# Performance work log

Hardware: AMD Instinct MI355X
Metric: run time of the kernel (lower is better)

Reference implementation:

```python
import jax, jax.numpy as jnp
import numpy as np

IN_F = 8192
OUT_F = 8192
MAX_STATES = 100
THRESHOLD = MAX_STATES // 2  # 50


def setup_inputs() -> dict:
    key = jax.random.key(0)
    k1, k2 = jax.random.split(key, 2)
    spike_input = (jax.random.uniform(k1, (IN_F,)) < 0.2).astype(jnp.float32)
    # synapse states as in __init__: randn*5 + threshold, clamped to [1, max_states]
    synapse_states = jnp.clip(
        jax.random.normal(k2, (OUT_F, IN_F)) * 5.0 + THRESHOLD, 1.0, float(MAX_STATES)
    ).astype(jnp.float32)
    membrane_potential = jnp.zeros((OUT_F,), jnp.float32)
    adaptive_threshold = jnp.full((OUT_F,), 3.0, jnp.float32)
    eligibility_trace = jnp.zeros((OUT_F, IN_F), jnp.float32)
    refractory_period = jnp.zeros((OUT_F,), jnp.float32)
    return {
        "spike_input": spike_input,
        "synapse_states": synapse_states,
        "membrane_potential": membrane_potential,
        "adaptive_threshold": adaptive_threshold,
        "eligibility_trace": eligibility_trace,
        "refractory_period": refractory_period,
    }


def reference(spike_input, synapse_states, membrane_potential, adaptive_threshold,
              eligibility_trace, refractory_period):
    # Ternary (effectively binary 0/1) weights from synapse states
    w = (synapse_states > float(THRESHOLD)).astype(jnp.float32)  # [out, in]
    x = spike_input.reshape(-1)                                   # [in]
    current = w @ x                                               # [out]
    # LIF membrane update with refractory gating
    v_mem = membrane_potential * 0.5 + current * (1.0 - refractory_period * 0.5)
    spikes = (v_mem >= adaptive_threshold).astype(jnp.float32)    # [out]
    # Eligibility trace: decay + outer-product accumulation + clamp
    new_trace = jnp.clip(eligibility_trace * 0.8 + jnp.outer(spikes, x), 0.0, 5.0)
    # Refractory update
    new_refractory = jnp.clip(refractory_period + spikes - 0.1, 0.0, 1.0)
    # Membrane reset where spiked
    new_membrane = v_mem * (1.0 - spikes)
    return spikes, new_membrane, new_trace, new_refractory
```

## Files before the change

### kernel.cpp

```cpp
#include <hip/hip_runtime.h>


#define IN_F 8192
#define OUT_F 8192
#define BLOCK 256

__global__ __launch_bounds__(BLOCK) void snn_matvec_kernel(
    const float4* __restrict__ x4,
    const float* __restrict__ syn,
    const float* __restrict__ mem,
    const float* __restrict__ thr,
    const float* __restrict__ refr,
    float* __restrict__ out_spikes,
    float* __restrict__ out_mem,
    float* __restrict__ out_refr)
{
    const int wave = threadIdx.x >> 6;
    const int lane = threadIdx.x & 63;
    const int row  = (blockIdx.x << 2) + wave;

    const float4* __restrict__ syn4 =
        (const float4*)(syn + (size_t)row * IN_F);

    float acc = 0.0f;
    #pragma unroll 8
    for (int it = 0; it < IN_F / 4 / 64; ++it) {
        const int idx = (it << 6) + lane;
        const float4 s  = syn4[idx];
        const float4 xv = x4[idx];
        acc += (s.x > 50.0f) ? xv.x : 0.0f;
        acc += (s.y > 50.0f) ? xv.y : 0.0f;
        acc += (s.z > 50.0f) ? xv.z : 0.0f;
        acc += (s.w > 50.0f) ? xv.w : 0.0f;
    }
    #pragma unroll
    for (int off = 32; off > 0; off >>= 1) {
        acc += __shfl_down(acc, off, 64);
    }
    if (lane == 0) {
        const float r = refr[row];
        const float v = mem[row] * 0.5f + acc * (1.0f - r * 0.5f);
        const float spike = (v >= thr[row]) ? 1.0f : 0.0f;
        out_spikes[row] = spike;
        out_mem[row]    = v * (1.0f - spike);
        out_refr[row]   = fminf(fmaxf(r + spike - 0.1f, 0.0f), 1.0f);
    }
}

__global__ __launch_bounds__(BLOCK) void snn_trace_kernel(
    const float4* __restrict__ x4,
    const float4* __restrict__ tr4,
    const float* __restrict__ spikes,
    float4* __restrict__ otr4)
{
    const int row = blockIdx.x;
    const float spike = spikes[row];
    const size_t base = (size_t)row * (IN_F / 4);

    #pragma unroll
    for (int it = 0; it < IN_F / 4 / BLOCK; ++it) {
        const int idx = it * BLOCK + threadIdx.x;
        const float4 t  = tr4[base + idx];
        const float4 xv = x4[idx];
        float4 o;
        o.x = fminf(fmaxf(t.x * 0.8f + spike * xv.x, 0.0f), 5.0f);
        o.y = fminf(fmaxf(t.y * 0.8f + spike * xv.y, 0.0f), 5.0f);
        o.z = fminf(fmaxf(t.z * 0.8f + spike * xv.z, 0.0f), 5.0f);
        o.w = fminf(fmaxf(t.w * 0.8f + spike * xv.w, 0.0f), 5.0f);
        otr4[base + idx] = o;
    }
}

extern "C" void kernel_launch(void* const* d_in, const int* in_sizes, int n_in,
                              void* d_out, int out_size, void* d_ws, size_t ws_size,
                              hipStream_t stream) {
    const float* x_in  = (const float*)d_in[0];
    const float* syn   = (const float*)d_in[1];
    const float* mem   = (const float*)d_in[2];
    const float* thr   = (const float*)d_in[3];
    const float* trace = (const float*)d_in[4];
    const float* refr  = (const float*)d_in[5];

    float* out = (float*)d_out;
    float* out_spikes = out;
    float* out_mem    = out + OUT_F;
    float* out_trace  = out + 2 * OUT_F;
    float* out_refr   = out + 2 * OUT_F + (size_t)OUT_F * IN_F;

    snn_matvec_kernel<<<OUT_F / 4, BLOCK, 0, stream>>>(
        (const float4*)x_in, syn, mem, thr, refr,
        out_spikes, out_mem, out_refr);

    snn_trace_kernel<<<OUT_F, BLOCK, 0, stream>>>(
        (const float4*)x_in, (const float4*)trace, out_spikes,
        (float4*)out_trace);
}
```

Measured before the change: 589.6 us.

## Fuse matvec and eligibility-trace update into one kernel with nontemporal accesses

Merges the spike matvec and the trace update into a single kernel in which each wave computes its row's spike, then immediately streams that row's trace. An xor-shuffle reduction gives every lane the spike value, removing the second launch and the global spike round-trip. Synapse and trace streams use nontemporal loads and stores to avoid cache pollution. Each wave now does twice the sequential work, which may reduce memory-level parallelism per row.

```diff
diff --git a/kernel.cpp b/kernel.cpp
--- a/kernel.cpp
+++ b/kernel.cpp
@@ -4,70 +4,68 @@
 #define IN_F 8192
 #define OUT_F 8192
 #define BLOCK 256
+#define CHUNKS (IN_F / 4 / 64)
 
-__global__ __launch_bounds__(BLOCK) void snn_matvec_kernel(
-    const float4* __restrict__ x4,
+typedef float f32x4 __attribute__((ext_vector_type(4)));
+
+__global__ __launch_bounds__(BLOCK) void snn_fused_kernel(
+    const f32x4* __restrict__ x4,
     const float* __restrict__ syn,
     const float* __restrict__ mem,
     const float* __restrict__ thr,
     const float* __restrict__ refr,
+    const f32x4* __restrict__ tr4,
     float* __restrict__ out_spikes,
     float* __restrict__ out_mem,
-    float* __restrict__ out_refr)
+    float* __restrict__ out_refr,
+    f32x4* __restrict__ otr4)
 {
     const int wave = threadIdx.x >> 6;
     const int lane = threadIdx.x & 63;
     const int row  = (blockIdx.x << 2) + wave;
 
-    const float4* __restrict__ syn4 =
-        (const float4*)(syn + (size_t)row * IN_F);
+    const size_t base4 = (size_t)row * (IN_F / 4);
+    const f32x4* __restrict__ syn4 = (const f32x4*)syn + base4;
+
+    const float r_in = refr[row];
+    const float m_in = mem[row];
+    const float t_in = thr[row];
 
     float acc = 0.0f;
     #pragma unroll 8
-    for (int it = 0; it < IN_F / 4 / 64; ++it) {
+    for (int it = 0; it < CHUNKS; ++it) {
         const int idx = (it << 6) + lane;
-        const float4 s  = syn4[idx];
-        const float4 xv = x4[idx];
-        acc += (s.x > 50.0f) ? xv.x : 0.0f;
-        acc += (s.y > 50.0f) ? xv.y : 0.0f;
-        acc += (s.z > 50.0f) ? xv.z : 0.0f;
-        acc += (s.w > 50.0f) ? xv.w : 0.0f;
+        const f32x4 s  = __builtin_nontemporal_load(&syn4[idx]);
+        const f32x4 xv = x4[idx];
+        acc += (s[0] > 50.0f) ? xv[0] : 0.0f;
+        acc += (s[1] > 50.0f) ? xv[1] : 0.0f;
+        acc += (s[2] > 50.0f) ? xv[2] : 0.0f;
+        acc += (s[3] > 50.0f) ? xv[3] : 0.0f;
     }
+
     #pragma unroll
-    for (int off = 32; off > 0; off >>= 1) {
-        acc += __shfl_down(acc, off, 64);
-    }
+    for (int off = 32; off > 0; off >>= 1)
+        acc += __shfl_xor(acc, off, 64);
+
+    const float v     = m_in * 0.5f + acc * (1.0f - r_in * 0.5f);
+    const float spike = (v >= t_in) ? 1.0f : 0.0f;
     if (lane == 0) {
-        const float r = refr[row];
-        const float v = mem[row] * 0.5f + acc * (1.0f - r * 0.5f);
-        const float spike = (v >= thr[row]) ? 1.0f : 0.0f;
         out_spikes[row] = spike;
         out_mem[row]    = v * (1.0f - spike);
-        out_refr[row]   = fminf(fmaxf(r + spike - 0.1f, 0.0f), 1.0f);
+        out_refr[row]   = fminf(fmaxf(r_in + spike - 0.1f, 0.0f), 1.0f);
     }
-}
 
-__global__ __launch_bounds__(BLOCK) void snn_trace_kernel(
-    const float4* __restrict__ x4,
-    const float4* __restrict__ tr4,
-    const float* __restrict__ spikes,
-    float4* __restrict__ otr4)
-{
-    const int row = blockIdx.x;
-    const float spike = spikes[row];
-    const size_t base = (size_t)row * (IN_F / 4);
-
-    #pragma unroll
-    for (int it = 0; it < IN_F / 4 / BLOCK; ++it) {
-        const int idx = it * BLOCK + threadIdx.x;
-        const float4 t  = tr4[base + idx];
-        const float4 xv = x4[idx];
-        float4 o;
-        o.x = fminf(fmaxf(t.x * 0.8f + spike * xv.x, 0.0f), 5.0f);
-        o.y = fminf(fmaxf(t.y * 0.8f + spike * xv.y, 0.0f), 5.0f);
-        o.z = fminf(fmaxf(t.z * 0.8f + spike * xv.z, 0.0f), 5.0f);
-        o.w = fminf(fmaxf(t.w * 0.8f + spike * xv.w, 0.0f), 5.0f);
-        otr4[base + idx] = o;
+    #pragma unroll 8
+    for (int it = 0; it < CHUNKS; ++it) {
+        const int idx = (it << 6) + lane;
+        const f32x4 t  = __builtin_nontemporal_load(&tr4[base4 + idx]);
+        const f32x4 xv = x4[idx];
+        f32x4 o;
+        o[0] = fminf(fmaxf(t[0] * 0.8f + spike * xv[0], 0.0f), 5.0f);
+        o[1] = fminf(fmaxf(t[1] * 0.8f + spike * xv[1], 0.0f), 5.0f);
+        o[2] = fminf(fmaxf(t[2] * 0.8f + spike * xv[2], 0.0f), 5.0f);
+        o[3] = fminf(fmaxf(t[3] * 0.8f + spike * xv[3], 0.0f), 5.0f);
+        __builtin_nontemporal_store(o, &otr4[base4 + idx]);
     }
 }
 
@@ -87,11 +85,9 @@
     float* out_trace  = out + 2 * OUT_F;
     float* out_refr   = out + 2 * OUT_F + (size_t)OUT_F * IN_F;
 
-    snn_matvec_kernel<<<OUT_F / 4, BLOCK, 0, stream>>>(
-        (const float4*)x_in, syn, mem, thr, refr,
-        out_spikes, out_mem, out_refr);
-
-    snn_trace_kernel<<<OUT_F, BLOCK, 0, stream>>>(
-        (const float4*)x_in, (const float4*)trace, out_spikes,
-        (float4*)out_trace);
+    snn_fused_kernel<<<OUT_F / 4, BLOCK, 0, stream>>>(
+        (const f32x4*)x_in, syn, mem, thr, refr,
+        (const f32x4*)trace,
+        out_spikes, out_mem, out_refr,
+        (f32x4*)out_trace);
 }
```

New measurement: 578.4 us. About the same (-1.9%).
